# Optimization experiments

Hardware: AMD Instinct MI355X
Metric: run time of the kernel (lower is better)

Reference implementation:

```python
import jax, jax.numpy as jnp
import numpy as np

# ---- model dims (match init_kwargs) ----
HIDDEN = 2048
N_HEADS = 16
Q_LORA = 768
KV_LORA = 512
NOPE = 128
ROPE = 64
V_DIM = 128
QK_HEAD = NOPE + ROPE  # 192
EPS = 1e-6


def _rms_norm(x, w):
    var = jnp.mean(jnp.square(x), axis=-1, keepdims=True)
    return x * jax.lax.rsqrt(var + EPS) * w


def _rotate_half(x):
    x1, x2 = jnp.split(x, 2, axis=-1)
    return jnp.concatenate([-x2, x1], axis=-1)


def _apply_rotary(x, cos, sin):
    # x: (b, h, s, d_r); cos/sin: (b, s, d_r) -> broadcast over heads
    c = cos[:, None, :, :]
    s = sin[:, None, :, :]
    return x * c + _rotate_half(x) * s


def setup_inputs() -> dict:
    key = jax.random.key(0)
    ks = jax.random.split(key, 8)
    B, S = 2, 2048

    hidden_states = jax.random.normal(ks[0], (B, S, HIDDEN), dtype=jnp.float32)

    # proper rotary cos/sin tables on the decoupled rope sub-dimension
    inv_freq = 1.0 / (10000.0 ** (np.arange(0, ROPE, 2, dtype=np.float32) / ROPE))
    pos = np.arange(S, dtype=np.float32)
    ang = np.einsum('s,d->sd', pos, inv_freq)           # (S, ROPE/2)
    emb = np.concatenate([ang, ang], axis=-1)           # (S, ROPE)
    cos = jnp.broadcast_to(jnp.asarray(np.cos(emb)), (B, S, ROPE)).astype(jnp.float32)
    sin = jnp.broadcast_to(jnp.asarray(np.sin(emb)), (B, S, ROPE)).astype(jnp.float32)

    # causal additive mask (1,1,S,S)
    neg = jnp.finfo(jnp.float32).min
    causal = jnp.where(jnp.tril(jnp.ones((S, S), dtype=bool)), 0.0, neg)
    attention_mask = causal[None, None, :, :]

    sd = 0.02
    wq_a = jax.random.normal(ks[1], (Q_LORA, HIDDEN), dtype=jnp.float32) * sd
    q_norm_w = jnp.ones((Q_LORA,), dtype=jnp.float32)
    wq_b = jax.random.normal(ks[2], (N_HEADS * QK_HEAD, Q_LORA), dtype=jnp.float32) * sd
    wkv_a = jax.random.normal(ks[3], (KV_LORA + ROPE, HIDDEN), dtype=jnp.float32) * sd
    kv_norm_w = jnp.ones((KV_LORA,), dtype=jnp.float32)
    wkv_b = jax.random.normal(ks[4], (N_HEADS * (NOPE + V_DIM), KV_LORA), dtype=jnp.float32) * sd
    wo = jax.random.normal(ks[5], (HIDDEN, N_HEADS * V_DIM), dtype=jnp.float32) * sd

    return dict(hidden_states=hidden_states, cos=cos, sin=sin,
                attention_mask=attention_mask, wq_a=wq_a, q_norm_w=q_norm_w,
                wq_b=wq_b, wkv_a=wkv_a, kv_norm_w=kv_norm_w, wkv_b=wkv_b, wo=wo)


def reference(hidden_states, cos, sin, attention_mask,
              wq_a, q_norm_w, wq_b, wkv_a, kv_norm_w, wkv_b, wo):
    B, S, _ = hidden_states.shape
    scaling = QK_HEAD ** -0.5

    # low-rank query projection: down -> RMSNorm -> up
    q = _rms_norm(hidden_states @ wq_a.T, q_norm_w) @ wq_b.T   # (B,S,H*QK_HEAD)
    q = q.reshape(B, S, N_HEADS, QK_HEAD).transpose(0, 2, 1, 3)  # (B,H,S,QK_HEAD)
    q_nope, q_pe = q[..., :NOPE], q[..., NOPE:]
    q_pe = _apply_rotary(q_pe, cos, sin)                        # (B,H,S,ROPE)

    # low-rank kv projection: latent + decoupled rope key
    kv_full = hidden_states @ wkv_a.T                           # (B,S,KV_LORA+ROPE)
    kv_lat, k_pe = kv_full[..., :KV_LORA], kv_full[..., KV_LORA:]
    k_pe = _apply_rotary(k_pe[:, None, :, :], cos, sin)         # (B,1,S,ROPE)

    # matrix absorption: fold wkv_b's k-part into q_nope
    wkv_b_h = wkv_b.reshape(N_HEADS, NOPE + V_DIM, KV_LORA)     # (H, NOPE+V, C)
    q_lat = jnp.einsum('bhsd,hdc->bhsc', q_nope, wkv_b_h[:, :NOPE])  # (B,H,S,C)

    kv = _rms_norm(kv_lat, kv_norm_w)[:, None, :, :]            # (B,1,S,C)

    # attention scores against the latent cache + rope key
    attn = (jnp.einsum('bhsc,bktc->bhst', q_lat, kv) +
            jnp.einsum('bhsr,bktr->bhst', q_pe, k_pe)) * scaling  # (B,H,S,S)
    attn = attn + attention_mask[:, :, :, :S]
    attn_weights = jax.nn.softmax(attn.astype(jnp.float32), axis=-1).astype(q_lat.dtype)

    # aggregate latent values, then absorb wkv_b's v-part
    ctx = jnp.einsum('bhst,bktc->bhsc', attn_weights, kv)       # (B,H,S,C)
    out = jnp.einsum('bhsc,hdc->bhsd', ctx, wkv_b_h[:, NOPE:])  # (B,H,S,V)
    out = out.transpose(0, 2, 1, 3).reshape(B, S, N_HEADS * V_DIM)
    attn_output = out @ wo.T                                    # (B,S,HIDDEN)
    return attn_output, attn_weights
```

## Files before the change

### kernel.cpp

```cpp
#include <hip/hip_runtime.h>
#include <stdint.h>

#define S_LEN   2048
#define B_SZ    2
#define HIDDEN  2048
#define N_HEADS 16
#define Q_LORA  768
#define KV_LORA 512
#define NOPE    128
#define ROPE    64
#define V_DIM   128
#define QK_HEAD 192
#define KEXT    576
#define EPSV    1e-6f
#define QKC_LD  1344

#define TRI_Z   2228224

typedef __attribute__((ext_vector_type(8))) short bf16x8;
typedef __attribute__((ext_vector_type(4))) float f32x4;

__device__ __forceinline__ unsigned short f2bf(float f){
  union { float f; unsigned u; } v; v.f = f;
  unsigned u = v.u;
  return (unsigned short)((u + 0x7FFFu + ((u >> 16) & 1u)) >> 16);
}
__device__ __forceinline__ float bf2f(unsigned short h){
  union { unsigned u; float f; } v; v.u = ((unsigned)h) << 16; return v.f;
}

__device__ __forceinline__ void gload16(const unsigned short* g, unsigned short* l){
  __builtin_amdgcn_global_load_lds((const __attribute__((address_space(1))) void*)g,
                                   (__attribute__((address_space(3))) void*)l, 16, 0, 0);
}

#define C_HS   2097152
#define C_WQA  (C_HS   + 393216)
#define C_WQB  (C_WQA  + 589824)
#define C_WKVA (C_WQB  + 294912)
#define C_WKVB (C_WKVA + 524288)
#define C_WO   (C_WKVB + 1048576)
__global__ void cast_all(const float* __restrict__ hs, const float* __restrict__ wqa,
                         const float* __restrict__ wqb, const float* __restrict__ wkva,
                         const float* __restrict__ wkvb, const float* __restrict__ wo,
                         unsigned short* __restrict__ d_hs, unsigned short* __restrict__ d_wqa,
                         unsigned short* __restrict__ d_wqb, unsigned short* __restrict__ d_wkva,
                         unsigned short* __restrict__ d_wkvb, unsigned short* __restrict__ d_wo){
  int i = blockIdx.x * blockDim.x + threadIdx.x;
  const float* s; unsigned short* d; int j;
  if      (i < C_HS)   { s = hs;   d = d_hs;   j = i; }
  else if (i < C_WQA)  { s = wqa;  d = d_wqa;  j = i - C_HS; }
  else if (i < C_WQB)  { s = wqb;  d = d_wqb;  j = i - C_WQA; }
  else if (i < C_WKVA) { s = wkva; d = d_wkva; j = i - C_WQB; }
  else if (i < C_WKVB) { s = wkvb; d = d_wkvb; j = i - C_WKVA; }
  else if (i < C_WO)   { s = wo;   d = d_wo;   j = i - C_WKVB; }
  else return;
  float4 v = ((const float4*)s)[j];
  ushort4 o;
  o.x = f2bf(v.x); o.y = f2bf(v.y); o.z = f2bf(v.z); o.w = f2bf(v.w);
  ((ushort4*)d)[j] = o;
}

__global__ void transpose_tile(const unsigned short* __restrict__ in, unsigned short* __restrict__ out,
                               int ldin, long inStride, int ldout, long outStride){
  __shared__ unsigned short t[64][65];
  int r0 = blockIdx.y * 64, c0 = blockIdx.x * 64;
  const unsigned short* ib = in + (long)blockIdx.z * inStride;
  unsigned short* ob = out + (long)blockIdx.z * outStride;
  int tid = threadIdx.x;
  #pragma unroll
  for (int i = 0; i < 16; i++) {
    int idx = i * 256 + tid;
    int lr = idx >> 6, lc = idx & 63;
    t[lr][lc] = ib[(long)(r0 + lr) * ldin + c0 + lc];
  }
  __syncthreads();
  #pragma unroll
  for (int i = 0; i < 16; i++) {
    int idx = i * 256 + tid;
    int lr = idx >> 6, lc = idx & 63;
    ob[(long)(c0 + lr) * ldout + r0 + lc] = t[lc][lr];
  }
}

template<bool C_F32, bool TRI_A, bool SKIP_UPPER>
__launch_bounds__(256)
__global__ void gemm_kernel(const unsigned short* __restrict__ A, const unsigned short* __restrict__ B,
                            void* __restrict__ Cv,
                            int M, int N, int K, int lda, int ldb, int ldc,
                            long strideA, long strideB,
                            int adiv, int amod,
                            int bdiv, int bmod,
                            int cdiv, long cstride1, int cmod, long cstride2,
                            float alpha)
{
  if (SKIP_UPPER && blockIdx.x > blockIdx.y) return;

  __shared__ __align__(16) unsigned short As[2*128*32];
  __shared__ __align__(16) unsigned short Bs[2*128*32];

  int z  = blockIdx.z;
  int m0 = blockIdx.y * 128;
  int n0 = blockIdx.x * 128;
  int idxA = (z / adiv) % amod;
  int idxB = (z / bdiv) % bmod;
  const unsigned short* Bb = B + (long)idxB * strideB;
  long cOff = (long)(z / cdiv) * cstride1 + (long)(z % cmod) * cstride2;

  int kmax = TRI_A ? (m0 + 128) : K;
  long aBase;
  if (TRI_A) {
    int rt = m0 >> 7;
    aBase = (long)idxA * strideA + (long)(rt * (rt + 1) / 2) * 16384;
  } else {
    aBase = (long)idxA * strideA;
  }

  int tid  = threadIdx.x;
  int lane = tid & 63;
  int wid  = tid >> 6;
  int wm   = (wid & 1) * 64;
  int wn   = (wid >> 1) * 64;
  int lrow = lane & 15;
  int kgrp = lane >> 4;

  int sR = wid * 16 + (lane >> 2);
  int sC = (lane & 3) * 8;
  int aStr = TRI_A ? kmax : lda;
  const unsigned short* aP = A + aBase + (TRI_A ? 0L : (long)m0 * lda) + (long)sR * aStr + sC;
  const unsigned short* bP = Bb + (long)(n0 + sR) * ldb + sC;
  unsigned short* ldsA = &As[wid * 512];
  unsigned short* ldsB = &Bs[wid * 512];

  f32x4 zero = {0.f, 0.f, 0.f, 0.f};
  f32x4 acc[4][4];
  #pragma unroll
  for (int i = 0; i < 4; i++)
    #pragma unroll
    for (int j = 0; j < 4; j++) acc[i][j] = zero;

  for (int k0 = 0; k0 < kmax; k0 += 64) {
    gload16(aP + k0,                             ldsA);
    gload16(aP + (long)64 * aStr + k0,           ldsA + 2048);
    gload16(aP + (k0 + 32),                      ldsA + 4096);
    gload16(aP + (long)64 * aStr + (k0 + 32),    ldsA + 4096 + 2048);
    gload16(bP + k0,                             ldsB);
    gload16(bP + (long)64 * ldb + k0,            ldsB + 2048);
    gload16(bP + (k0 + 32),                      ldsB + 4096);
    gload16(bP + (long)64 * ldb + (k0 + 32),     ldsB + 4096 + 2048);
    __syncthreads();

    #pragma unroll
    for (int kk = 0; kk < 2; kk++) {
      bf16x8 af[4], bfg[4];
      #pragma unroll
      for (int mt = 0; mt < 4; mt++)
        af[mt] = *(const bf16x8*)&As[kk*4096 + (wm + mt*16 + lrow)*32 + kgrp*8];
      #pragma unroll
      for (int nt = 0; nt < 4; nt++)
        bfg[nt] = *(const bf16x8*)&Bs[kk*4096 + (wn + nt*16 + lrow)*32 + kgrp*8];
      #pragma unroll
      for (int mt = 0; mt < 4; mt++)
        #pragma unroll
        for (int nt = 0; nt < 4; nt++)
          acc[mt][nt] = __builtin_amdgcn_mfma_f32_16x16x32_bf16(af[mt], bfg[nt], acc[mt][nt], 0, 0, 0);
    }
    __syncthreads();
  }

  #pragma unroll
  for (int mt = 0; mt < 4; mt++) {
    #pragma unroll
    for (int nt = 0; nt < 4; nt++) {
      int col = n0 + wn + nt*16 + lrow;
      if (col >= N) continue;
      int rowb = m0 + wm + mt*16 + kgrp*4;
      #pragma unroll
      for (int r = 0; r < 4; r++) {
        int row = rowb + r;
        if (row >= M) continue;
        float v = acc[mt][nt][r] * alpha;
        if (C_F32) ((float*)Cv)[cOff + (long)row * ldc + col] = v;
        else ((unsigned short*)Cv)[cOff + (long)row * ldc + col] = f2bf(v);
      }
    }
  }
}

__global__ void rmsnorm_q(const float* __restrict__ in, const float* __restrict__ w,
                          unsigned short* __restrict__ out){
  __shared__ float red[4];
  int row = blockIdx.x;
  const float* x = in + (size_t)row * QKC_LD;
  int tid = threadIdx.x;
  float v0 = x[tid], v1 = x[tid + 256], v2 = x[tid + 512];
  float s = v0*v0 + v1*v1 + v2*v2;
  #pragma unroll
  for (int o = 32; o > 0; o >>= 1) s += __shfl_xor(s, o, 64);
  int lane = tid & 63, wid = tid >> 6;
  if (lane == 0) red[wid] = s;
  __syncthreads();
  float tot = red[0] + red[1] + red[2] + red[3];
  float r = rsqrtf(tot * (1.0f / Q_LORA) + EPSV);
  unsigned short* op = out + (size_t)row * Q_LORA;
  op[tid]       = f2bf(v0 * r * w[tid]);
  op[tid + 256] = f2bf(v1 * r * w[tid + 256]);
  op[tid + 512] = f2bf(v2 * r * w[tid + 512]);
}

__global__ void kv_prep(const float* __restrict__ qkc, const float* __restrict__ w,
                        const float* __restrict__ cosb, const float* __restrict__ sinb,
                        unsigned short* __restrict__ kext){
  __shared__ float red[4];
  int row = blockIdx.x;
  const float* x = qkc + (size_t)row * QKC_LD + Q_LORA;
  int tid = threadIdx.x;
  float v0 = x[tid], v1 = x[tid + 256];
  float s = v0*v0 + v1*v1;
  #pragma unroll
  for (int o = 32; o > 0; o >>= 1) s += __shfl_xor(s, o, 64);
  int lane = tid & 63, wid = tid >> 6;
  if (lane == 0) red[wid] = s;
  __syncthreads();
  float tot = red[0] + red[1] + red[2] + red[3];
  float r = rsqrtf(tot * (1.0f / KV_LORA) + EPSV);
  unsigned short* op = kext + (size_t)row * KEXT;
  op[tid]       = f2bf(v0 * r * w[tid]);
  op[tid + 256] = f2bf(v1 * r * w[tid + 256]);
  if (tid < 64) {
    int i = tid;
    float xi = x[512 + i];
    float other = (i < 32) ? -x[512 + i + 32] : x[512 + i - 32];
    float c  = cosb[(size_t)row * 64 + i];
    float sn = sinb[(size_t)row * 64 + i];
    op[512 + i] = f2bf(xi * c + other * sn);
  }
}

__global__ void q_prep(const unsigned short* __restrict__ qfull, const float* __restrict__ cosb,
                       const float* __restrict__ sinb, unsigned short* __restrict__ qnope,
                       unsigned short* __restrict__ qext){
  int row = blockIdx.x;
  int h   = blockIdx.y;
  int b   = row >> 11;
  int s_  = row & 2047;
  const unsigned short* x = qfull + (size_t)row * (N_HEADS * QK_HEAD) + h * QK_HEAD;
  int tid = threadIdx.x;
  long base = ((long)(b * N_HEADS + h) * S_LEN + s_);
  if (tid < 128) {
    qnope[base * NOPE + tid] = x[tid];
  } else {
    int i = tid - 128;
    float xi = bf2f(x[128 + i]);
    float other = (i < 32) ? -bf2f(x[128 + i + 32]) : bf2f(x[128 + i - 32]);
    float c  = cosb[(size_t)row * 64 + i];
    float sn = sinb[(size_t)row * 64 + i];
    qext[base * KEXT + 512 + i] = f2bf(xi * c + other * sn);
  }
}

__global__ void softmax_rows(float* __restrict__ scores, unsigned short* __restrict__ probs){
  __shared__ float red[4];
  int gid = blockIdx.x;
  int z = gid >> 11;
  int r = gid & 2047;
  float* x = scores + (size_t)gid * S_LEN;
  int rt = r >> 7;
  int rowlen = (rt + 1) << 7;
  unsigned short* prow = probs + (long)z * TRI_Z + (long)(rt * (rt + 1) / 2) * 16384
                         + (long)(r - (rt << 7)) * rowlen;
  int tid = threadIdx.x;
  float v[8];
  #pragma unroll
  for (int i = 0; i < 8; i++) {
    int idx = tid + i * 256;
    v[i] = (idx <= r) ? x[idx] : -3.4028234663852886e38f;
  }
  float m = v[0];
  #pragma unroll
  for (int i = 1; i < 8; i++) m = fmaxf(m, v[i]);
  #pragma unroll
  for (int o = 32; o > 0; o >>= 1) m = fmaxf(m, __shfl_xor(m, o, 64));
  int lane = tid & 63, wid = tid >> 6;
  if (lane == 0) red[wid] = m;
  __syncthreads();
  m = fmaxf(fmaxf(red[0], red[1]), fmaxf(red[2], red[3]));
  __syncthreads();
  float s = 0.f;
  #pragma unroll
  for (int i = 0; i < 8; i++) {
    int idx = tid + i * 256;
    v[i] = (idx <= r) ? __expf(v[i] - m) : 0.f;
    s += v[i];
  }
  #pragma unroll
  for (int o = 32; o > 0; o >>= 1) s += __shfl_xor(s, o, 64);
  if (lane == 0) red[wid] = s;
  __syncthreads();
  s = red[0] + red[1] + red[2] + red[3];
  float inv = 1.0f / s;
  #pragma unroll
  for (int i = 0; i < 8; i++) {
    int idx = tid + i * 256;
    float p = v[i] * inv;
    x[idx] = p;
    if (idx < rowlen) prow[idx] = f2bf(p);
  }
}

extern "C" void kernel_launch(void* const* d_in, const int* in_sizes, int n_in,
                              void* d_out, int out_size, void* d_ws, size_t ws_size,
                              hipStream_t stream) {
  const float* hs    = (const float*)d_in[0];
  const float* cosb  = (const float*)d_in[1];
  const float* sinb  = (const float*)d_in[2];
  const float* wq_a  = (const float*)d_in[4];
  const float* q_nw  = (const float*)d_in[5];
  const float* wq_b  = (const float*)d_in[6];
  const float* wkv_a = (const float*)d_in[7];
  const float* kv_nw = (const float*)d_in[8];
  const float* wkv_b = (const float*)d_in[9];
  const float* wo    = (const float*)d_in[10];

  float* attn_out = (float*)d_out;
  float* scores   = attn_out + (size_t)B_SZ * S_LEN * HIDDEN;

  char* ws = (char*)d_ws;
  const size_t o_wkvb  = 0;
  const size_t o_wo    = 4194304;
  const size_t AR      = 16777216;
  const size_t o_wqa   = AR + 0;
  const size_t o_wkva  = AR + 3145728;
  const size_t o_wqb   = AR + 5505024;
  const size_t o_wkvbT = AR + 10223616;
  const size_t o_hs    = AR + 12320768;
  const size_t o_qkc   = AR + 29097984;
  const size_t o_qn    = AR + 51118080;
  const size_t o_qfull = AR + 57409536;
  const size_t o_kext  = AR + 82575360;
  const size_t o_qnope = AR + 87293952;
  const size_t o_qext  = AR + 104071168;
  const size_t o_probs = AR + 0;
  const size_t o_vwT   = AR + 142606336;
  const size_t o_outc  = AR + 176160768;
  const size_t total   = AR + 192937984;
  if (ws_size < total) return;

  unsigned short* wkvb_bf = (unsigned short*)(ws + o_wkvb);
  unsigned short* wo_bf   = (unsigned short*)(ws + o_wo);
  unsigned short* wqa_bf  = (unsigned short*)(ws + o_wqa);
  unsigned short* wkva_bf = (unsigned short*)(ws + o_wkva);
  unsigned short* wqb_bf  = (unsigned short*)(ws + o_wqb);
  unsigned short* wkvbT   = (unsigned short*)(ws + o_wkvbT);
  unsigned short* hs_bf   = (unsigned short*)(ws + o_hs);
  float*          qkc     = (float*)(ws + o_qkc);
  unsigned short* qn      = (unsigned short*)(ws + o_qn);
  unsigned short* qfull   = (unsigned short*)(ws + o_qfull);
  unsigned short* kext    = (unsigned short*)(ws + o_kext);
  unsigned short* qnope   = (unsigned short*)(ws + o_qnope);
  unsigned short* qext    = (unsigned short*)(ws + o_qext);
  unsigned short* probs   = (unsigned short*)(ws + o_probs);
  unsigned short* vwT     = (unsigned short*)(ws + o_vwT);
  unsigned short* outcat  = (unsigned short*)(ws + o_outc);

  cast_all<<<dim3((C_WO + 255) / 256), dim3(256), 0, stream>>>(
      hs, wq_a, wq_b, wkv_a, wkv_b, wo,
      hs_bf, wqa_bf, wqb_bf, wkva_bf, wkvb_bf, wo_bf);

  transpose_tile<<<dim3(8,2,16),256,0,stream>>>(wkvb_bf, wkvbT, 512, 131072L, 128, 65536L);

  gemm_kernel<true,false,false><<<dim3(11,32,1),256,0,stream>>>(
      hs_bf, wqa_bf, qkc, 4096, 1344, 2048, 2048, 2048, QKC_LD,
      0L, 0L, 1, 1, 1, 1, 1, 0L, 1, 0L, 1.0f);
  rmsnorm_q<<<dim3(4096),dim3(256),0,stream>>>(qkc, q_nw, qn);
  kv_prep<<<dim3(4096),dim3(256),0,stream>>>(qkc, kv_nw, cosb, sinb, kext);
  gemm_kernel<false,false,false><<<dim3(24,32,1),256,0,stream>>>(
      qn, wqb_bf, qfull, 4096, 3072, 768, 768, 768, 3072,
      0L, 0L, 1, 1, 1, 1, 1, 0L, 1, 0L, 1.0f);
  q_prep<<<dim3(4096,16),dim3(192),0,stream>>>(qfull, cosb, sinb, qnope, qext);
  gemm_kernel<false,false,false><<<dim3(4,16,32),256,0,stream>>>(
      qnope, wkvbT, qext, 2048, 512, 128, 128, 128, 576,
      262144L, 65536L, 1, 1000000, 1, 16, 1, 1179648L, 1, 0L, 1.0f);
  gemm_kernel<true,false,true><<<dim3(16,16,32),256,0,stream>>>(
      qext, kext, scores, 2048, 2048, 576, 576, 576, 2048,
      1179648L, 1179648L, 1, 1000000, 16, 1000000, 1, 4194304L, 1, 0L,
      0.07216878364870322f);
  gemm_kernel<false,false,false><<<dim3(16,1,32),256,0,stream>>>(
      wkvb_bf + 65536, kext, vwT, 128, 2048, 512, 512, KEXT, 2048,
      131072L, 1179648L, 1, 16, 16, 2, 1, 262144L, 1, 0L, 1.0f);
  softmax_rows<<<dim3(65536),dim3(256),0,stream>>>(scores, probs);
  gemm_kernel<false,true,false><<<dim3(1,16,32),256,0,stream>>>(
      probs, vwT, outcat, 2048, 128, 2048, 0, 2048, 2048,
      (long)TRI_Z, 262144L, 1, 1000000, 1, 1000000, 16, 4194304L, 16, 128L, 1.0f);
  gemm_kernel<true,false,false><<<dim3(16,32,1),256,0,stream>>>(
      outcat, wo_bf, attn_out, 4096, 2048, 2048, 2048, 2048, 2048,
      0L, 0L, 1, 1, 1, 1, 1, 0L, 1, 0L, 1.0f);
}
```

Baseline: 1.212 ms.

## Double-buffer LDS tiles in GEMM to overlap global loads with MFMA

The GEMM kernel now keeps two shared-memory stages for A and B. It issues the direct-to-LDS loads for tile k+1 before computing tile k, and uses explicit vmcnt waits and raw barriers instead of __syncthreads. The goal is to hide global-load latency behind the MFMA work. In exchange, LDS use per block doubles, which can reduce occupancy, and correctness now depends on the hand-written waitcnt counts matching the number of loads in flight.

```diff
diff --git a/kernel.cpp b/kernel.cpp
--- a/kernel.cpp
+++ b/kernel.cpp
@@ -96,8 +96,8 @@
 {
   if (SKIP_UPPER && blockIdx.x > blockIdx.y) return;
 
-  __shared__ __align__(16) unsigned short As[2*128*32];
-  __shared__ __align__(16) unsigned short Bs[2*128*32];
+  __shared__ __align__(16) unsigned short As[2*128*64];
+  __shared__ __align__(16) unsigned short Bs[2*128*64];
 
   int z  = blockIdx.z;
   int m0 = blockIdx.y * 128;
@@ -129,8 +129,19 @@
   int aStr = TRI_A ? kmax : lda;
   const unsigned short* aP = A + aBase + (TRI_A ? 0L : (long)m0 * lda) + (long)sR * aStr + sC;
   const unsigned short* bP = Bb + (long)(n0 + sR) * ldb + sC;
-  unsigned short* ldsA = &As[wid * 512];
-  unsigned short* ldsB = &Bs[wid * 512];
+
+  auto stage = [&](int buf, int k0){
+    unsigned short* lA = &As[buf * 8192 + wid * 512];
+    unsigned short* lB = &Bs[buf * 8192 + wid * 512];
+    gload16(aP + k0,                          lA);
+    gload16(aP + (long)64 * aStr + k0,        lA + 2048);
+    gload16(aP + (k0 + 32),                   lA + 4096);
+    gload16(aP + (long)64 * aStr + (k0 + 32), lA + 4096 + 2048);
+    gload16(bP + k0,                          lB);
+    gload16(bP + (long)64 * ldb + k0,         lB + 2048);
+    gload16(bP + (k0 + 32),                   lB + 4096);
+    gload16(bP + (long)64 * ldb + (k0 + 32),  lB + 4096 + 2048);
+  };
 
   f32x4 zero = {0.f, 0.f, 0.f, 0.f};
   f32x4 acc[4][4];
@@ -139,33 +150,38 @@
     #pragma unroll
     for (int j = 0; j < 4; j++) acc[i][j] = zero;
 
-  for (int k0 = 0; k0 < kmax; k0 += 64) {
-    gload16(aP + k0,                             ldsA);
-    gload16(aP + (long)64 * aStr + k0,           ldsA + 2048);
-    gload16(aP + (k0 + 32),                      ldsA + 4096);
-    gload16(aP + (long)64 * aStr + (k0 + 32),    ldsA + 4096 + 2048);
-    gload16(bP + k0,                             ldsB);
-    gload16(bP + (long)64 * ldb + k0,            ldsB + 2048);
-    gload16(bP + (k0 + 32),                      ldsB + 4096);
-    gload16(bP + (long)64 * ldb + (k0 + 32),     ldsB + 4096 + 2048);
-    __syncthreads();
-
+  int nk = kmax >> 6;
+  stage(0, 0);
+
+  for (int t = 0; t < nk; t++) {
+    int cur = t & 1;
+    if (t + 1 < nk) {
+      stage(cur ^ 1, (t + 1) << 6);
+      asm volatile("s_waitcnt vmcnt(8)" ::: "memory");
+    } else {
+      asm volatile("s_waitcnt vmcnt(0)" ::: "memory");
+    }
+    asm volatile("s_barrier" ::: "memory");
+
+    const unsigned short* Ab = &As[cur * 8192];
+    const unsigned short* Bt = &Bs[cur * 8192];
     #pragma unroll
     for (int kk = 0; kk < 2; kk++) {
       bf16x8 af[4], bfg[4];
       #pragma unroll
       for (int mt = 0; mt < 4; mt++)
-        af[mt] = *(const bf16x8*)&As[kk*4096 + (wm + mt*16 + lrow)*32 + kgrp*8];
+        af[mt] = *(const bf16x8*)&Ab[kk*4096 + (wm + mt*16 + lrow)*32 + kgrp*8];
       #pragma unroll
       for (int nt = 0; nt < 4; nt++)
-        bfg[nt] = *(const bf16x8*)&Bs[kk*4096 + (wn + nt*16 + lrow)*32 + kgrp*8];
+        bfg[nt] = *(const bf16x8*)&Bt[kk*4096 + (wn + nt*16 + lrow)*32 + kgrp*8];
       #pragma unroll
       for (int mt = 0; mt < 4; mt++)
         #pragma unroll
         for (int nt = 0; nt < 4; nt++)
           acc[mt][nt] = __builtin_amdgcn_mfma_f32_16x16x32_bf16(af[mt], bfg[nt], acc[mt][nt], 0, 0, 0);
     }
-    __syncthreads();
+    asm volatile("s_waitcnt lgkmcnt(0)" ::: "memory");
+    asm volatile("s_barrier" ::: "memory");
   }
 
   #pragma unroll
```

Result: slower. 1.249 ms (+3.1%).
